# Optimization experiments

Measured on AMD Instinct MI355X. Metric: run time of the kernel, lower is better.

The kernel has to match this reference:

```python
import jax, jax.numpy as jnp
import numpy as np

V, E, H, A, L = 32000, 512, 1024, 512, 2  # vocab, embed, hidden, attn, n_layers
B, S = 64, 128


def setup_inputs() -> dict:
    key = jax.random.key(0)
    ks = jax.random.split(key, 20)
    sc = 0.02
    inp = {
        "token": jax.random.randint(ks[0], (B,), 0, V),
        "hidden": jax.random.normal(ks[1], (L, B, H), jnp.float32),
        "cell": jax.random.normal(ks[2], (L, B, H), jnp.float32),
        "enc_out": jax.random.normal(ks[3], (S, B, 2 * H), jnp.float32),
        "emb_table": (jax.random.normal(ks[4], (V, E), jnp.float32) * sc).at[0].set(0.0),  # padding_idx=0
        "W_enc": jax.random.normal(ks[5], (A, 2 * H), jnp.float32) * sc,
        "W_dec": jax.random.normal(ks[6], (A, H), jnp.float32) * sc,
        "v_w": jax.random.normal(ks[7], (A,), jnp.float32) * sc,
        "W_ih0": jax.random.normal(ks[8], (4 * H, E + 2 * H), jnp.float32) * sc,
        "W_hh0": jax.random.normal(ks[9], (4 * H, H), jnp.float32) * sc,
        "b_ih0": jax.random.normal(ks[10], (4 * H,), jnp.float32) * sc,
        "b_hh0": jax.random.normal(ks[11], (4 * H,), jnp.float32) * sc,
        "W_ih1": jax.random.normal(ks[12], (4 * H, H), jnp.float32) * sc,
        "W_hh1": jax.random.normal(ks[13], (4 * H, H), jnp.float32) * sc,
        "b_ih1": jax.random.normal(ks[14], (4 * H,), jnp.float32) * sc,
        "b_hh1": jax.random.normal(ks[15], (4 * H,), jnp.float32) * sc,
        "fc_W": jax.random.normal(ks[16], (V, 3 * H), jnp.float32) * sc,
        "fc_b": jax.random.normal(ks[17], (V,), jnp.float32) * sc,
    }
    return inp


def _lstm_cell(x, h, c, W_ih, W_hh, b_ih, b_hh):
    # PyTorch gate order: i, f, g, o
    gates = x @ W_ih.T + h @ W_hh.T + (b_ih + b_hh)  # (B, 4H)
    i, f, g, o = jnp.split(gates, 4, axis=-1)
    i, f, o = jax.nn.sigmoid(i), jax.nn.sigmoid(f), jax.nn.sigmoid(o)
    c_new = f * c + i * jnp.tanh(g)
    h_new = o * jnp.tanh(c_new)
    return h_new, c_new


def reference(token, hidden, cell, enc_out, emb_table, W_enc, W_dec, v_w,
              W_ih0, W_hh0, b_ih0, b_hh0, W_ih1, W_hh1, b_ih1, b_hh1, fc_W, fc_b):
    embedded = emb_table[token]                      # (B, E)
    top = hidden[-1]                                 # (B, H)
    enc_t = jnp.transpose(enc_out, (1, 0, 2))        # (B, S, 2H)
    # additive attention: v . tanh(W_enc enc + W_dec s_t)
    energy = jnp.tanh(jnp.einsum('bsd,ad->bsa', enc_t, W_enc)
                      + (top @ W_dec.T)[:, None, :])  # (B, S, A)
    score = jnp.einsum('bsa,a->bs', energy, v_w)     # (B, S)
    alpha = jax.nn.softmax(score, axis=-1)           # (B, S)
    context = jnp.einsum('bs,bsd->bd', alpha, enc_t)  # (B, 2H)
    x0 = jnp.concatenate([embedded, context], axis=-1)  # (B, E+2H)
    h0, c0 = _lstm_cell(x0, hidden[0], cell[0], W_ih0, W_hh0, b_ih0, b_hh0)
    h1, c1 = _lstm_cell(h0, hidden[1], cell[1], W_ih1, W_hh1, b_ih1, b_hh1)
    logits = jnp.concatenate([h1, context], axis=-1) @ fc_W.T + fc_b  # (B, V)
    new_hidden = jnp.stack([h0, h1], axis=0)
    new_cell = jnp.stack([c0, c1], axis=0)
    return logits, new_hidden, new_cell, alpha
```

## Files before the change

kernel.cpp:

```cpp
#include <hip/hip_runtime.h>
#include <stdint.h>

#define HD    1024
#define BATCH 64
#define SEQ   128
#define AD    512
#define EMBD  512
#define VOCAB 32000

typedef float f32x4 __attribute__((ext_vector_type(4)));
typedef short bf8   __attribute__((ext_vector_type(8)));

#define WS_SCOREP 0
#define WS_DECP   32768
#define WS_G0     65536
#define WS_G1     1114112
#define WS_LCTX   2162688
#define WS_X0BF   4210688
#define WS_XFCBF  4292608
#define WS_HIDBF  4390912
#define WS_WENCBF 4456448
#define WS_H0BF   4980736

#define OUT_LOGITS 0
#define OUT_HID    2048000
#define OUT_CELL   2179072
#define OUT_ALPHA  2310144

__device__ __forceinline__ short f2bf(float f) {
  uint32_t u = __float_as_uint(f);
  u += 0x7FFF + ((u >> 16) & 1);
  return (short)(u >> 16);
}

__device__ __forceinline__ void store_bf4(short* p, float4 v) {
  short4 s;
  s.x = f2bf(v.x); s.y = f2bf(v.y); s.z = f2bf(v.z); s.w = f2bf(v.w);
  *(short4*)p = s;
}

__device__ __forceinline__ void gemm_f32A(
    short (*As)[72], short (*Bs)[72],
    const float* __restrict__ A, int lda,
    const float* __restrict__ Bm, int ldb, int K_total, int n0,
    float* __restrict__ C, int ldc, const float* __restrict__ bias) {
  const int tid = threadIdx.x;
  const int wave = tid >> 6, lane = tid & 63;
  const int quad = lane >> 4, l16 = lane & 15;
  const int srow = tid >> 4, sc4 = (tid & 15) * 4;

  f32x4 acc[4];
#pragma unroll
  for (int i = 0; i < 4; ++i) acc[i] = (f32x4){0.f, 0.f, 0.f, 0.f};

  float4 pa[4], pb[4];
#pragma unroll
  for (int p = 0; p < 4; ++p) {
    int row = srow + p * 16;
    pa[p] = *(const float4*)&A[(size_t)row * lda + sc4];
    pb[p] = *(const float4*)&Bm[(size_t)(n0 + row) * ldb + sc4];
  }

  for (int kt = 0; kt < K_total; kt += 64) {
#pragma unroll
    for (int p = 0; p < 4; ++p) {
      int row = srow + p * 16;
      store_bf4(&As[row][sc4], pa[p]);
      store_bf4(&Bs[row][sc4], pb[p]);
    }
    __syncthreads();
    if (kt + 64 < K_total) {
      int kn = kt + 64;
#pragma unroll
      for (int p = 0; p < 4; ++p) {
        int row = srow + p * 16;
        pa[p] = *(const float4*)&A[(size_t)row * lda + kn + sc4];
        pb[p] = *(const float4*)&Bm[(size_t)(n0 + row) * ldb + kn + sc4];
      }
    }
#pragma unroll
    for (int kk = 0; kk < 64; kk += 32) {
      bf8 af = *(const bf8*)&As[wave * 16 + l16][kk + quad * 8];
#pragma unroll
      for (int ns = 0; ns < 4; ++ns) {
        bf8 bq = *(const bf8*)&Bs[ns * 16 + l16][kk + quad * 8];
        acc[ns] = __builtin_amdgcn_mfma_f32_16x16x32_bf16(af, bq, acc[ns], 0, 0, 0);
      }
    }
    __syncthreads();
  }

#pragma unroll
  for (int ns = 0; ns < 4; ++ns) {
    int n = n0 + ns * 16 + l16;
    float bv = bias ? bias[n] : 0.f;
#pragma unroll
    for (int r = 0; r < 4; ++r) {
      int m = wave * 16 + quad * 4 + r;
      C[(size_t)m * ldc + n] = acc[ns][r] + bv;
    }
  }
}

__device__ __forceinline__ void gemm_bf16A(
    short (*As)[72], short (*Bs)[72],
    const short* __restrict__ A1, int lda1, int K1,
    const float* __restrict__ B1, int ldb1,
    const short* __restrict__ A2, int lda2,
    const float* __restrict__ B2, int ldb2,
    int t0, int ntiles, int n0,
    float* __restrict__ C, int ldc,
    const float* __restrict__ bias,
    const float* __restrict__ Cadd, int ldadd) {
  const int tid = threadIdx.x;
  const int wave = tid >> 6, lane = tid & 63;
  const int quad = lane >> 4, l16 = lane & 15;
  const int arow = tid >> 3, ac8 = (tid & 7) * 8;
  const int brow = tid >> 4, bc4 = (tid & 15) * 4;

  f32x4 acc[4];
#pragma unroll
  for (int i = 0; i < 4; ++i) acc[i] = (f32x4){0.f, 0.f, 0.f, 0.f};

  bf8 qa[2];
  float4 pb[4];
  auto loadAB = [&](int tile) {
    int kv = tile * 64;
    const short* Ap; const float* Bp; int la, lb, ko;
    if (kv < K1) { Ap = A1; Bp = B1; la = lda1; lb = ldb1; ko = kv; }
    else         { Ap = A2; Bp = B2; la = lda2; lb = ldb2; ko = kv - K1; }
#pragma unroll
    for (int p = 0; p < 2; ++p)
      qa[p] = *(const bf8*)&Ap[(size_t)(arow + p * 32) * la + ko + ac8];
#pragma unroll
    for (int p = 0; p < 4; ++p)
      pb[p] = *(const float4*)&Bp[(size_t)(n0 + brow + p * 16) * lb + ko + bc4];
  };

  loadAB(t0);
  for (int ti = t0; ti < t0 + ntiles; ++ti) {
#pragma unroll
    for (int p = 0; p < 2; ++p) *(bf8*)&As[arow + p * 32][ac8] = qa[p];
#pragma unroll
    for (int p = 0; p < 4; ++p) store_bf4(&Bs[brow + p * 16][bc4], pb[p]);
    __syncthreads();
    if (ti + 1 < t0 + ntiles) loadAB(ti + 1);
#pragma unroll
    for (int kk = 0; kk < 64; kk += 32) {
      bf8 af = *(const bf8*)&As[wave * 16 + l16][kk + quad * 8];
#pragma unroll
      for (int ns = 0; ns < 4; ++ns) {
        bf8 bq = *(const bf8*)&Bs[ns * 16 + l16][kk + quad * 8];
        acc[ns] = __builtin_amdgcn_mfma_f32_16x16x32_bf16(af, bq, acc[ns], 0, 0, 0);
      }
    }
    __syncthreads();
  }

#pragma unroll
  for (int ns = 0; ns < 4; ++ns) {
    int n = n0 + ns * 16 + l16;
    float bv = bias ? bias[n] : 0.f;
#pragma unroll
    for (int r = 0; r < 4; ++r) {
      int m = wave * 16 + quad * 4 + r;
      float v = acc[ns][r] + bv;
      if (Cadd) v += Cadd[(size_t)m * ldadd + n];
      C[(size_t)m * ldc + n] = v;
    }
  }
}

__global__ __launch_bounds__(256) void k_prep(
    float* __restrict__ ws, const int* __restrict__ token,
    const float* __restrict__ emb, const float* __restrict__ hidden,
    const float* __restrict__ Wenc, const float* __restrict__ Wdec) {
  __shared__ __align__(16) short As[64][72];
  __shared__ __align__(16) short Bs[64][72];
  const int bx = blockIdx.x, t = threadIdx.x;
  if (bx < 8) {
    gemm_f32A(As, Bs, hidden + BATCH * HD, HD, Wdec, HD, 1024, bx * 64,
              ws + WS_DECP, AD, nullptr);
    return;
  }
  if (bx < 40) {
    int idx = (bx - 8) * 256 + t;
    int b = idx >> 7, e4 = (idx & 127) * 4;
    int tok = token[b];
    float4 v = *(const float4*)&emb[(size_t)tok * EMBD + e4];
    store_bf4((short*)(ws + WS_X0BF) + (size_t)b * 2560 + e4, v);
    return;
  }
  if (bx < 168) {
    int idx = (bx - 40) * 256 + t;
    float4 v = *(const float4*)&hidden[(size_t)idx * 4];
    store_bf4((short*)(ws + WS_HIDBF) + (size_t)idx * 4, v);
    return;
  }
  int idx = (bx - 168) * 256 + t;
  size_t base = (size_t)idx * 8;
  float4 v0 = *(const float4*)&Wenc[base];
  float4 v1 = *(const float4*)&Wenc[base + 4];
  short* dst = (short*)(ws + WS_WENCBF) + base;
  store_bf4(dst, v0);
  store_bf4(dst + 4, v1);
}

__global__ __launch_bounds__(256) void k_attn(
    const float* __restrict__ enc, const short* __restrict__ wencbf,
    const float* __restrict__ dec_proj, const float* __restrict__ vw,
    float* __restrict__ scorep) {
  __shared__ __align__(16) short As[64][72];
  __shared__ __align__(16) short Bs[128][72];
  const int tid = threadIdx.x;
  const int wave = tid >> 6, lane = tid & 63;
  const int quad = lane >> 4, l16 = lane & 15;
  const int mblk = blockIdx.x, nblk = blockIdx.y;
  const int b = mblk >> 1, s0 = (mblk & 1) * 64;
  const int n0 = nblk * 128;
  const size_t abase = ((size_t)s0 * BATCH + b) * 2048;
  const int srow = tid >> 4, sc4 = (tid & 15) * 4;
  const int brow = tid >> 3, bc8 = (tid & 7) * 8;

  f32x4 acc[8];
#pragma unroll
  for (int i = 0; i < 8; ++i) acc[i] = (f32x4){0.f, 0.f, 0.f, 0.f};

  float4 pa[4];
  bf8 qb[4];
  auto loadAB = [&](int kt) {
#pragma unroll
    for (int p = 0; p < 4; ++p) {
      int row = srow + p * 16;
      pa[p] = *(const float4*)&enc[abase + (size_t)row * (BATCH * 2048) + kt + sc4];
    }
#pragma unroll
    for (int p = 0; p < 4; ++p)
      qb[p] = *(const bf8*)&wencbf[(size_t)(n0 + brow + p * 32) * 2048 + kt + bc8];
  };

  loadAB(0);
  for (int kt = 0; kt < 2048; kt += 64) {
#pragma unroll
    for (int p = 0; p < 4; ++p) store_bf4(&As[srow + p * 16][sc4], pa[p]);
#pragma unroll
    for (int p = 0; p < 4; ++p) *(bf8*)&Bs[brow + p * 32][bc8] = qb[p];
    __syncthreads();
    if (kt + 64 < 2048) loadAB(kt + 64);
#pragma unroll
    for (int kk = 0; kk < 64; kk += 32) {
      bf8 af = *(const bf8*)&As[wave * 16 + l16][kk + quad * 8];
#pragma unroll
      for (int ns = 0; ns < 8; ++ns) {
        bf8 bq = *(const bf8*)&Bs[ns * 16 + l16][kk + quad * 8];
        acc[ns] = __builtin_amdgcn_mfma_f32_16x16x32_bf16(af, bq, acc[ns], 0, 0, 0);
      }
    }
    __syncthreads();
  }

  float part[4] = {0.f, 0.f, 0.f, 0.f};
#pragma unroll
  for (int ns = 0; ns < 8; ++ns) {
    int n = n0 + ns * 16 + l16;
    float dp = dec_proj[b * AD + n];
    float vv = vw[n];
#pragma unroll
    for (int r = 0; r < 4; ++r) part[r] += tanhf(acc[ns][r] + dp) * vv;
  }
#pragma unroll
  for (int r = 0; r < 4; ++r) {
    float v = part[r];
    v += __shfl_xor(v, 1);
    v += __shfl_xor(v, 2);
    v += __shfl_xor(v, 4);
    v += __shfl_xor(v, 8);
    if (l16 == 0)
      scorep[nblk * (BATCH * SEQ) + mblk * 64 + wave * 16 + quad * 4 + r] = v;
  }
}

__global__ __launch_bounds__(256) void k_softmax_ctx(
    const float* __restrict__ scorep, const float* __restrict__ enc,
    float* __restrict__ alpha_out, short* __restrict__ x0bf,
    short* __restrict__ xfcbf) {
  const int b = blockIdx.x, dchunk = blockIdx.y, t = threadIdx.x;
  __shared__ float al[128];
  __shared__ float buf[128];
  float sv = 0.f;
  if (t < 128) {
    sv = scorep[b * SEQ + t] + scorep[8192 + b * SEQ + t]
       + scorep[16384 + b * SEQ + t] + scorep[24576 + b * SEQ + t];
    buf[t] = sv;
  }
  __syncthreads();
  for (int off = 64; off > 0; off >>= 1) {
    if (t < off) buf[t] = fmaxf(buf[t], buf[t + off]);
    __syncthreads();
  }
  float mx = buf[0];
  __syncthreads();
  float e = 0.f;
  if (t < 128) { e = __expf(sv - mx); buf[t] = e; }
  __syncthreads();
  for (int off = 64; off > 0; off >>= 1) {
    if (t < off) buf[t] += buf[t + off];
    __syncthreads();
  }
  float inv = 1.f / buf[0];
  if (t < 128) {
    float a = e * inv;
    al[t] = a;
    if (dchunk == 0) alpha_out[b * SEQ + t] = a;
  }
  __syncthreads();

  const int d = dchunk * 1024 + t * 4;
  float4 acc = make_float4(0.f, 0.f, 0.f, 0.f);
#pragma unroll 4
  for (int s = 0; s < SEQ; ++s) {
    float4 ev = *(const float4*)&enc[((size_t)s * BATCH + b) * 2048 + d];
    float w = al[s];
    acc.x += w * ev.x; acc.y += w * ev.y;
    acc.z += w * ev.z; acc.w += w * ev.w;
  }
  store_bf4(&x0bf[(size_t)b * 2560 + 512 + d], acc);
  store_bf4(&xfcbf[(size_t)b * 3072 + 1024 + d], acc);
}

__global__ __launch_bounds__(256) void k_big0(
    float* __restrict__ ws, const float* __restrict__ W_ih0,
    const float* __restrict__ W_hh0, const float* __restrict__ fc_W) {
  __shared__ __align__(16) short As[64][72];
  __shared__ __align__(16) short Bs[64][72];
  const short* x0bf   = (const short*)(ws + WS_X0BF);
  const short* hid0bf = (const short*)(ws + WS_HIDBF);
  const short* xfcbf  = (const short*)(ws + WS_XFCBF);
  int bx = blockIdx.x;
  if (bx < 500) {
    gemm_bf16A(As, Bs,
               xfcbf + 1024, 3072, 2048, fc_W + 1024, 3072,
               xfcbf + 1024, 3072, fc_W + 1024, 3072,
               0, 32, bx * 64,
               ws + WS_LCTX, VOCAB, nullptr, nullptr, 0);
  } else {
    int g = bx - 500;
    int nblk = g & 63, z = g >> 6;
    gemm_bf16A(As, Bs,
               x0bf, 2560, 2560, W_ih0, 2560,
               hid0bf, 1024, W_hh0, 1024,
               z * 14, 14, nblk * 64,
               ws + WS_G0 + (size_t)z * (64 * 4096), 4096, nullptr, nullptr, 0);
  }
}

__global__ __launch_bounds__(256) void k_gates1(
    float* __restrict__ ws, const float* __restrict__ W_ih1,
    const float* __restrict__ W_hh1) {
  __shared__ __align__(16) short As[64][72];
  __shared__ __align__(16) short Bs[64][72];
  const short* h0bf   = (const short*)(ws + WS_H0BF);
  const short* hid1bf = (const short*)(ws + WS_HIDBF) + BATCH * HD;
  int nblk = blockIdx.x & 63, z = blockIdx.x >> 6;
  gemm_bf16A(As, Bs,
             h0bf, 1024, 1024, W_ih1, 1024,
             hid1bf, 1024, W_hh1, 1024,
             z * 8, 8, nblk * 64,
             ws + WS_G1 + (size_t)z * (64 * 4096), 4096, nullptr, nullptr, 0);
}

__global__ __launch_bounds__(256) void k_fc_h1(
    float* __restrict__ ws, const float* __restrict__ fc_W,
    const float* __restrict__ fc_b, float* __restrict__ out_logits) {
  __shared__ __align__(16) short As[64][72];
  __shared__ __align__(16) short Bs[64][72];
  const short* xfcbf = (const short*)(ws + WS_XFCBF);
  gemm_bf16A(As, Bs,
             xfcbf, 3072, 1024, fc_W, 3072,
             xfcbf, 3072, fc_W, 3072,
             0, 16, blockIdx.x * 64,
             out_logits, VOCAB, fc_b, ws + WS_LCTX, VOCAB);
}

__global__ __launch_bounds__(256) void k_act(
    const float* __restrict__ gslab,
    const float* __restrict__ b_ih, const float* __restrict__ b_hh,
    const float* __restrict__ cell_in,
    float* __restrict__ hid_out, float* __restrict__ cell_out,
    short* __restrict__ hbf, int hstride) {
  int idx = blockIdx.x * 256 + threadIdx.x;
  int b = idx >> 10, n = idx & 1023;
  float gi = b_ih[n]        + b_hh[n];
  float gf = b_ih[1024 + n] + b_hh[1024 + n];
  float gg = b_ih[2048 + n] + b_hh[2048 + n];
  float go = b_ih[3072 + n] + b_hh[3072 + n];
#pragma unroll
  for (int sl = 0; sl < 4; ++sl) {
    const float* g = gslab + (size_t)sl * (64 * 4096) + (size_t)b * 4096;
    gi += g[n];
    gf += g[1024 + n];
    gg += g[2048 + n];
    go += g[3072 + n];
  }
  float i = 1.f / (1.f + __expf(-gi));
  float f = 1.f / (1.f + __expf(-gf));
  float o = 1.f / (1.f + __expf(-go));
  float c = f * cell_in[idx] + i * tanhf(gg);
  float h = o * tanhf(c);
  cell_out[idx] = c;
  hid_out[idx] = h;
  hbf[(size_t)b * hstride + n] = f2bf(h);
}

extern "C" void kernel_launch(void* const* d_in, const int* in_sizes, int n_in,
                              void* d_out, int out_size, void* d_ws, size_t ws_size,
                              hipStream_t stream) {
  const int*   token  = (const int*)d_in[0];
  const float* hidden = (const float*)d_in[1];
  const float* cell   = (const float*)d_in[2];
  const float* enc    = (const float*)d_in[3];
  const float* emb    = (const float*)d_in[4];
  const float* W_enc  = (const float*)d_in[5];
  const float* W_dec  = (const float*)d_in[6];
  const float* v_w    = (const float*)d_in[7];
  const float* W_ih0  = (const float*)d_in[8];
  const float* W_hh0  = (const float*)d_in[9];
  const float* b_ih0  = (const float*)d_in[10];
  const float* b_hh0  = (const float*)d_in[11];
  const float* W_ih1  = (const float*)d_in[12];
  const float* W_hh1  = (const float*)d_in[13];
  const float* b_ih1  = (const float*)d_in[14];
  const float* b_hh1  = (const float*)d_in[15];
  const float* fc_W   = (const float*)d_in[16];
  const float* fc_b   = (const float*)d_in[17];

  float* out = (float*)d_out;
  float* ws  = (float*)d_ws;

  k_prep<<<680, 256, 0, stream>>>(ws, token, emb, hidden, W_enc, W_dec);

  k_attn<<<dim3(128, 4), 256, 0, stream>>>(
      enc, (const short*)(ws + WS_WENCBF), ws + WS_DECP, v_w, ws + WS_SCOREP);

  k_softmax_ctx<<<dim3(64, 2), 256, 0, stream>>>(
      ws + WS_SCOREP, enc, out + OUT_ALPHA,
      (short*)(ws + WS_X0BF), (short*)(ws + WS_XFCBF));

  k_big0<<<756, 256, 0, stream>>>(ws, W_ih0, W_hh0, fc_W);

  k_act<<<256, 256, 0, stream>>>(ws + WS_G0, b_ih0, b_hh0, cell,
                                 out + OUT_HID, out + OUT_CELL,
                                 (short*)(ws + WS_H0BF), HD);

  k_gates1<<<256, 256, 0, stream>>>(ws, W_ih1, W_hh1);

  k_act<<<256, 256, 0, stream>>>(ws + WS_G1, b_ih1, b_hh1, cell + BATCH * HD,
                                 out + OUT_HID + BATCH * HD,
                                 out + OUT_CELL + BATCH * HD,
                                 (short*)(ws + WS_XFCBF), 3072);

  k_fc_h1<<<500, 256, 0, stream>>>(ws, fc_W, fc_b, out + OUT_LOGITS);
}
```

Baseline: 750.7 us.

## Fuse LSTM layers and FC into one persistent kernel with atomic flag barriers

Merges the five post-attention launches (gates0, act0, gates1, act1, fc) into a single kernel. Blocks 0-255 run the LSTM chain separated by global atomic counters used as grid barriers, while blocks 256-755 compute the context part of the FC and then spin on a flag before adding the h1 part. This removes launch gaps and lets the context FC overlap the LSTM chain. It also remaps the attention grid to a 1D ordering, likely for cache locality. The spin barriers assume all 256 LSTM blocks are co-resident (launch_bounds 256,3), so deadlock is possible if they are not scheduled together.

Result: slower. 1.071 ms (+42.6%).

```diff
diff --git a/kernel.cpp b/kernel.cpp
--- a/kernel.cpp
+++ b/kernel.cpp
@@ -21,6 +21,7 @@
 #define WS_HIDBF  4390912
 #define WS_WENCBF 4456448
 #define WS_H0BF   4980736
+#define WS_FLAGS  5013504
 
 #define OUT_LOGITS 0
 #define OUT_HID    2048000
@@ -37,6 +38,21 @@
   short4 s;
   s.x = f2bf(v.x); s.y = f2bf(v.y); s.z = f2bf(v.z); s.w = f2bf(v.w);
   *(short4*)p = s;
+}
+
+__device__ __forceinline__ void sig(int* f) {
+  __threadfence();
+  __syncthreads();
+  if (threadIdx.x == 0)
+    __hip_atomic_fetch_add(f, 1, __ATOMIC_RELEASE, __HIP_MEMORY_SCOPE_AGENT);
+}
+__device__ __forceinline__ void waitf(int* f, int n) {
+  if (threadIdx.x == 0) {
+    while (__hip_atomic_load(f, __ATOMIC_RELAXED, __HIP_MEMORY_SCOPE_AGENT) < n)
+      __builtin_amdgcn_s_sleep(8);
+  }
+  __syncthreads();
+  __threadfence();
 }
 
 __device__ __forceinline__ void gemm_f32A(
@@ -171,6 +187,36 @@
   }
 }
 
+__device__ __forceinline__ void act_phase(
+    const float* __restrict__ gslab,
+    const float* __restrict__ b_ih, const float* __restrict__ b_hh,
+    const float* __restrict__ cell_in,
+    float* __restrict__ hid_out, float* __restrict__ cell_out,
+    short* __restrict__ hbf, int hstride, int blk) {
+  int idx = blk * 256 + threadIdx.x;
+  int b = idx >> 10, n = idx & 1023;
+  float gi = b_ih[n]        + b_hh[n];
+  float gf = b_ih[1024 + n] + b_hh[1024 + n];
+  float gg = b_ih[2048 + n] + b_hh[2048 + n];
+  float go = b_ih[3072 + n] + b_hh[3072 + n];
+#pragma unroll
+  for (int sl = 0; sl < 4; ++sl) {
+    const float* g = gslab + (size_t)sl * (64 * 4096) + (size_t)b * 4096;
+    gi += g[n];
+    gf += g[1024 + n];
+    gg += g[2048 + n];
+    go += g[3072 + n];
+  }
+  float i = 1.f / (1.f + __expf(-gi));
+  float f = 1.f / (1.f + __expf(-gf));
+  float o = 1.f / (1.f + __expf(-go));
+  float c = f * cell_in[idx] + i * tanhf(gg);
+  float h = o * tanhf(c);
+  cell_out[idx] = c;
+  hid_out[idx] = h;
+  hbf[(size_t)b * hstride + n] = f2bf(h);
+}
+
 __global__ __launch_bounds__(256) void k_prep(
     float* __restrict__ ws, const int* __restrict__ token,
     const float* __restrict__ emb, const float* __restrict__ hidden,
@@ -184,6 +230,7 @@
     return;
   }
   if (bx < 40) {
+    if (bx == 8 && t < 4) ((int*)(ws + WS_FLAGS))[t] = 0;
     int idx = (bx - 8) * 256 + t;
     int b = idx >> 7, e4 = (idx & 127) * 4;
     int tok = token[b];
@@ -215,7 +262,10 @@
   const int tid = threadIdx.x;
   const int wave = tid >> 6, lane = tid & 63;
   const int quad = lane >> 4, l16 = lane & 15;
-  const int mblk = blockIdx.x, nblk = blockIdx.y;
+  const int l = blockIdx.x;
+  const int s = l >> 3;
+  const int nblk = s & 3;
+  const int mblk = (l & 7) + (s >> 2) * 8;
   const int b = mblk >> 1, s0 = (mblk & 1) * 64;
   const int n0 = nblk * 128;
   const size_t abase = ((size_t)s0 * BATCH + b) * 2048;
@@ -328,88 +378,55 @@
   store_bf4(&xfcbf[(size_t)b * 3072 + 1024 + d], acc);
 }
 
-__global__ __launch_bounds__(256) void k_big0(
-    float* __restrict__ ws, const float* __restrict__ W_ih0,
-    const float* __restrict__ W_hh0, const float* __restrict__ fc_W) {
+__global__ __launch_bounds__(256, 3) void k_post(
+    float* __restrict__ ws,
+    const float* __restrict__ W_ih0, const float* __restrict__ W_hh0,
+    const float* __restrict__ b_ih0, const float* __restrict__ b_hh0,
+    const float* __restrict__ W_ih1, const float* __restrict__ W_hh1,
+    const float* __restrict__ b_ih1, const float* __restrict__ b_hh1,
+    const float* __restrict__ cell, const float* __restrict__ fc_W,
+    const float* __restrict__ fc_b, float* __restrict__ out) {
   __shared__ __align__(16) short As[64][72];
   __shared__ __align__(16) short Bs[64][72];
+  int* flags = (int*)(ws + WS_FLAGS);
   const short* x0bf   = (const short*)(ws + WS_X0BF);
   const short* hid0bf = (const short*)(ws + WS_HIDBF);
-  const short* xfcbf  = (const short*)(ws + WS_XFCBF);
-  int bx = blockIdx.x;
-  if (bx < 500) {
-    gemm_bf16A(As, Bs,
-               xfcbf + 1024, 3072, 2048, fc_W + 1024, 3072,
-               xfcbf + 1024, 3072, fc_W + 1024, 3072,
-               0, 32, bx * 64,
-               ws + WS_LCTX, VOCAB, nullptr, nullptr, 0);
+  const short* hid1bf = (const short*)(ws + WS_HIDBF) + BATCH * HD;
+  short* h0bf  = (short*)(ws + WS_H0BF);
+  short* xfcbf = (short*)(ws + WS_XFCBF);
+  const int bx = blockIdx.x;
+
+  if (bx < 256) {
+    const int nblk = bx & 63, z = bx >> 6;
+    gemm_bf16A(As, Bs, x0bf, 2560, 2560, W_ih0, 2560,
+               hid0bf, 1024, W_hh0, 1024, z * 14, 14, nblk * 64,
+               ws + WS_G0 + (size_t)z * (64 * 4096), 4096, nullptr, nullptr, 0);
+    sig(&flags[0]);
+    waitf(&flags[0], 256);
+    act_phase(ws + WS_G0, b_ih0, b_hh0, cell,
+              out + OUT_HID, out + OUT_CELL, h0bf, HD, bx);
+    sig(&flags[1]);
+    waitf(&flags[1], 256);
+    gemm_bf16A(As, Bs, (const short*)h0bf, 1024, 1024, W_ih1, 1024,
+               hid1bf, 1024, W_hh1, 1024, z * 8, 8, nblk * 64,
+               ws + WS_G1 + (size_t)z * (64 * 4096), 4096, nullptr, nullptr, 0);
+    sig(&flags[2]);
+    waitf(&flags[2], 256);
+    act_phase(ws + WS_G1, b_ih1, b_hh1, cell + BATCH * HD,
+              out + OUT_HID + BATCH * HD, out + OUT_CELL + BATCH * HD,
+              xfcbf, 3072, bx);
+    sig(&flags[3]);
   } else {
-    int g = bx - 500;
-    int nblk = g & 63, z = g >> 6;
-    gemm_bf16A(As, Bs,
-               x0bf, 2560, 2560, W_ih0, 2560,
-               hid0bf, 1024, W_hh0, 1024,
-               z * 14, 14, nblk * 64,
-               ws + WS_G0 + (size_t)z * (64 * 4096), 4096, nullptr, nullptr, 0);
-  }
-}
-
-__global__ __launch_bounds__(256) void k_gates1(
-    float* __restrict__ ws, const float* __restrict__ W_ih1,
-    const float* __restrict__ W_hh1) {
-  __shared__ __align__(16) short As[64][72];
-  __shared__ __align__(16) short Bs[64][72];
-  const short* h0bf   = (const short*)(ws + WS_H0BF);
-  const short* hid1bf = (const short*)(ws + WS_HIDBF) + BATCH * HD;
-  int nblk = blockIdx.x & 63, z = blockIdx.x >> 6;
-  gemm_bf16A(As, Bs,
-             h0bf, 1024, 1024, W_ih1, 1024,
-             hid1bf, 1024, W_hh1, 1024,
-             z * 8, 8, nblk * 64,
-             ws + WS_G1 + (size_t)z * (64 * 4096), 4096, nullptr, nullptr, 0);
-}
-
-__global__ __launch_bounds__(256) void k_fc_h1(
-    float* __restrict__ ws, const float* __restrict__ fc_W,
-    const float* __restrict__ fc_b, float* __restrict__ out_logits) {
-  __shared__ __align__(16) short As[64][72];
-  __shared__ __align__(16) short Bs[64][72];
-  const short* xfcbf = (const short*)(ws + WS_XFCBF);
-  gemm_bf16A(As, Bs,
-             xfcbf, 3072, 1024, fc_W, 3072,
-             xfcbf, 3072, fc_W, 3072,
-             0, 16, blockIdx.x * 64,
-             out_logits, VOCAB, fc_b, ws + WS_LCTX, VOCAB);
-}
-
-__global__ __launch_bounds__(256) void k_act(
-    const float* __restrict__ gslab,
-    const float* __restrict__ b_ih, const float* __restrict__ b_hh,
-    const float* __restrict__ cell_in,
-    float* __restrict__ hid_out, float* __restrict__ cell_out,
-    short* __restrict__ hbf, int hstride) {
-  int idx = blockIdx.x * 256 + threadIdx.x;
-  int b = idx >> 10, n = idx & 1023;
-  float gi = b_ih[n]        + b_hh[n];
-  float gf = b_ih[1024 + n] + b_hh[1024 + n];
-  float gg = b_ih[2048 + n] + b_hh[2048 + n];
-  float go = b_ih[3072 + n] + b_hh[3072 + n];
-#pragma unroll
-  for (int sl = 0; sl < 4; ++sl) {
-    const float* g = gslab + (size_t)sl * (64 * 4096) + (size_t)b * 4096;
-    gi += g[n];
-    gf += g[1024 + n];
-    gg += g[2048 + n];
-    go += g[3072 + n];
-  }
-  float i = 1.f / (1.f + __expf(-gi));
-  float f = 1.f / (1.f + __expf(-gf));
-  float o = 1.f / (1.f + __expf(-go));
-  float c = f * cell_in[idx] + i * tanhf(gg);
-  float h = o * tanhf(c);
-  cell_out[idx] = c;
-  hid_out[idx] = h;
-  hbf[(size_t)b * hstride + n] = f2bf(h);
+    const int j = bx - 256;
+    gemm_bf16A(As, Bs, (const short*)xfcbf + 1024, 3072, 2048, fc_W + 1024, 3072,
+               (const short*)xfcbf + 1024, 3072, fc_W + 1024, 3072,
+               0, 32, j * 64, ws + WS_LCTX, VOCAB, nullptr, nullptr, 0);
+    waitf(&flags[3], 256);
+    gemm_bf16A(As, Bs, (const short*)xfcbf, 3072, 1024, fc_W, 3072,
+               (const short*)xfcbf, 3072, fc_W, 3072,
+               0, 16, j * 64, out + OUT_LOGITS, VOCAB, fc_b,
+               ws + WS_LCTX, VOCAB);
+  }
 }
 
 extern "C" void kernel_launch(void* const* d_in, const int* in_sizes, int n_in,
@@ -439,25 +456,14 @@
 
   k_prep<<<680, 256, 0, stream>>>(ws, token, emb, hidden, W_enc, W_dec);
 
-  k_attn<<<dim3(128, 4), 256, 0, stream>>>(
+  k_attn<<<512, 256, 0, stream>>>(
       enc, (const short*)(ws + WS_WENCBF), ws + WS_DECP, v_w, ws + WS_SCOREP);
 
   k_softmax_ctx<<<dim3(64, 2), 256, 0, stream>>>(
       ws + WS_SCOREP, enc, out + OUT_ALPHA,
       (short*)(ws + WS_X0BF), (short*)(ws + WS_XFCBF));
 
-  k_big0<<<756, 256, 0, stream>>>(ws, W_ih0, W_hh0, fc_W);
-
-  k_act<<<256, 256, 0, stream>>>(ws + WS_G0, b_ih0, b_hh0, cell,
-                                 out + OUT_HID, out + OUT_CELL,
-                                 (short*)(ws + WS_H0BF), HD);
-
-  k_gates1<<<256, 256, 0, stream>>>(ws, W_ih1, W_hh1);
-
-  k_act<<<256, 256, 0, stream>>>(ws + WS_G1, b_ih1, b_hh1, cell + BATCH * HD,
-                                 out + OUT_HID + BATCH * HD,
-                                 out + OUT_CELL + BATCH * HD,
-                                 (short*)(ws + WS_XFCBF), 3072);
-
-  k_fc_h1<<<500, 256, 0, stream>>>(ws, fc_W, fc_b, out + OUT_LOGITS);
-}
+  k_post<<<756, 256, 0, stream>>>(
+      ws, W_ih0, W_hh0, b_ih0, b_hh0, W_ih1, W_hh1, b_ih1, b_hh1,
+      cell, fc_W, fc_b, out);
+}
```
